# Performance work log

Hardware: AMD Instinct MI355X
Metric: run time of the kernel (lower is better)

Reference implementation:

```python
import jax, jax.numpy as jnp
import numpy as np

B, S, T = 128, 128, 128
E, H = 256, 512
NEG_INF = -1e9


def setup_inputs() -> dict:
    key = jax.random.key(0)
    ks = jax.random.split(key, 12)
    rn = lambda k, sh: (jax.random.normal(k, sh, jnp.float32) * 0.05)
    return {
        "trg_embed": rn(ks[0], (B, T, E)),
        "encoder_hidden": rn(ks[1], (B, S, 2 * H)),
        "encoder_final": rn(ks[2], (1, B, 2 * H)),
        "src_mask": jnp.ones((B, 1, S), bool),
        "trg_mask": jnp.ones((B, T), bool),
        # Bahdanau attention params (Linear, bias=False)
        "W_key": rn(ks[3], (H, 2 * H)),      # key_layer
        "W_query": rn(ks[4], (H, H)),        # query_layer
        "v_energy": rn(ks[5], (H,)),         # energy_layer (H -> 1)
        # GRU cell params (torch layout: gates [r, z, n])
        "W_ih": rn(ks[6], (3 * H, E + 2 * H)),
        "W_hh": rn(ks[7], (3 * H, H)),
        "b_ih": rn(ks[8], (3 * H,)),
        "b_hh": rn(ks[9], (3 * H,)),
        # bridge: Linear(2H -> H, bias=True)
        "W_bridge": rn(ks[10], (H, 2 * H)),
        "b_bridge": jnp.zeros((H,), jnp.float32),
        # pre_output_layer: Linear(H + 2H + E -> H, bias=False)
        "W_preout": rn(ks[11], (H, H + 2 * H + E)),
    }


def reference(trg_embed, encoder_hidden, encoder_final, src_mask, trg_mask,
              W_key, W_query, v_energy, W_ih, W_hh, b_ih, b_hh,
              W_bridge, b_bridge, W_preout):
    # proj_key precomputed once, as in the torch module
    proj_key = jnp.einsum("bsk,hk->bsh", encoder_hidden, W_key)  # [B,S,H]
    # init_hidden: tanh(bridge(encoder_final)); num_layers=1 -> h: [B,H]
    h0 = jnp.tanh(encoder_final[0] @ W_bridge.T + b_bridge)
    mask = src_mask[:, 0, :]  # [B,S]

    def step(h, prev_embed):  # h: [B,H], prev_embed: [B,E]
        # Bahdanau additive attention, query = last-layer hidden
        q = h @ W_query.T  # [B,H]
        scores = jnp.einsum("bsh,h->bs", jnp.tanh(q[:, None, :] + proj_key), v_energy)
        scores = jnp.where(mask, scores, NEG_INF)
        alphas = jax.nn.softmax(scores, axis=-1)
        context = jnp.einsum("bs,bsd->bd", alphas, encoder_hidden)  # [B,2H]
        # single-step GRU (torch gate order r, z, n)
        x = jnp.concatenate([prev_embed, context], axis=-1)  # [B,E+2H]
        gi = x @ W_ih.T + b_ih
        gh = h @ W_hh.T + b_hh
        i_r, i_z, i_n = jnp.split(gi, 3, axis=-1)
        h_r, h_z, h_n = jnp.split(gh, 3, axis=-1)
        r = jax.nn.sigmoid(i_r + h_r)
        z = jax.nn.sigmoid(i_z + h_z)
        n = jnp.tanh(i_n + r * h_n)
        h_new = (1.0 - z) * n + z * h
        # pre-output projection (dropout p=0 / eval mode)
        pre = jnp.concatenate([prev_embed, h_new, context], axis=-1) @ W_preout.T
        return h_new, (h_new, pre)

    xs = jnp.swapaxes(trg_embed, 0, 1)  # [T,B,E]
    hT, (states, preouts) = jax.lax.scan(step, h0, xs)
    decoder_states = jnp.swapaxes(states, 0, 1)      # [B,T,H]
    pre_output_vectors = jnp.swapaxes(preouts, 0, 1)  # [B,T,H]
    hidden = hT[None]  # [1,B,H] to mirror torch layout
    cell_state = jnp.zeros_like(hidden)  # GRU: untouched zeros
    return decoder_states, hidden, pre_output_vectors, cell_state
```

## Files before the change

### kernel.cpp

```cpp
#include <hip/hip_runtime.h>
#include <hip/hip_bf16.h>

typedef __bf16 bf16_t;
typedef __bf16 bf16x8 __attribute__((ext_vector_type(8)));
typedef float  f32x4  __attribute__((ext_vector_type(4)));
typedef float  f32x2  __attribute__((ext_vector_type(2)));

#define Bx 128
#define Sx 128
#define Tx 128
#define Ex 256
#define Hx 512
#define H2 1024
#define G3 1536
#define KX 1280
#define KP 1792

#define OUT_STATES 0
#define OUT_HID    8388608
#define OUT_PRE    8454144
#define OUT_CELL   16842752

__device__ __forceinline__ float fast_tanh(float x){
  float e = __expf(2.0f*x);
  return 1.0f - 2.0f/(e + 1.0f);
}
__device__ __forceinline__ float fast_sigmoid(float x){
  return 1.0f/(1.0f + __expf(-x));
}

__device__ __forceinline__ bf16x8 ld_cvt8(const float* p){
  f32x4 a = *(const f32x4*)p;
  f32x4 b = *(const f32x4*)(p+4);
  bf16x8 r;
  r[0]=(bf16_t)a[0]; r[1]=(bf16_t)a[1]; r[2]=(bf16_t)a[2]; r[3]=(bf16_t)a[3];
  r[4]=(bf16_t)b[0]; r[5]=(bf16_t)b[1]; r[6]=(bf16_t)b[2]; r[7]=(bf16_t)b[3];
  return r;
}

__device__ __forceinline__ f32x4 gemm_tile_bb(const bf16_t* A, int lda,
                                              const bf16_t* W, int ldw, int K, int lane){
  const int quad = lane >> 4, c = lane & 15;
  const bf16_t* pa = A + c*lda + quad*8;
  const bf16_t* pb = W + c*ldw + quad*8;
  f32x4 acc = {0.f,0.f,0.f,0.f};
  for (int k = 0; k < K; k += 32)
    acc = __builtin_amdgcn_mfma_f32_16x16x32_bf16(*(const bf16x8*)(pa+k),
                                                  *(const bf16x8*)(pb+k), acc, 0, 0, 0);
  return acc;
}

__device__ __forceinline__ void store_tile_f32(float* C, int ldc, f32x4 acc, int lane){
  const int quad = lane >> 4, c = lane & 15;
  #pragma unroll
  for (int r = 0; r < 4; r++) C[(quad*4 + r)*ldc + c] = acc[r];
}

__global__ void cvt_kernel(const float* __restrict__ in, bf16_t* __restrict__ out, int n){
  const int i = (blockIdx.x*256 + threadIdx.x)*4;
  if (i < n){
    f32x4 v = *(const f32x4*)(in + i);
    bf16_t o[4]; o[0]=(bf16_t)v[0]; o[1]=(bf16_t)v[1]; o[2]=(bf16_t)v[2]; o[3]=(bf16_t)v[3];
    *(ulong1*)(out + i) = *(ulong1*)o;
  }
}

__global__ void bridge_kernel(const float* __restrict__ ef, const float* __restrict__ Wb,
                              const float* __restrict__ bb,
                              float* __restrict__ hf, bf16_t* __restrict__ hb){
  const int b = blockIdx.x;
  const int h = threadIdx.x;
  __shared__ float efs[H2];
  for (int k = threadIdx.x; k < H2; k += blockDim.x) efs[k] = ef[b*H2 + k];
  __syncthreads();
  const float* wrow = Wb + h*H2;
  float acc = bb[h];
  for (int k = 0; k < H2; k += 4){
    f32x4 w = *(const f32x4*)(wrow + k);
    acc += efs[k]*w[0] + efs[k+1]*w[1] + efs[k+2]*w[2] + efs[k+3]*w[3];
  }
  float v = fast_tanh(acc);
  hf[b*Hx + h] = v;
  hb[b*Hx + h] = (bf16_t)v;
}

__global__ void pk_gemm(const float* __restrict__ eh, const bf16_t* __restrict__ Wkb,
                        bf16_t* __restrict__ pk){
  const int gwid = (blockIdx.x*blockDim.x + threadIdx.x) >> 6;
  const int lane = threadIdx.x & 63;
  const int quad = lane >> 4, c = lane & 15;
  const int mt = gwid >> 5;
  const int nt = gwid & 31;
  const float*  pa = eh  + (mt*16 + c)*H2 + quad*8;
  const bf16_t* pb = Wkb + (nt*16 + c)*H2 + quad*8;
  f32x4 acc = {0.f,0.f,0.f,0.f};
  for (int k = 0; k < H2; k += 32)
    acc = __builtin_amdgcn_mfma_f32_16x16x32_bf16(ld_cvt8(pa + k),
                                                  *(const bf16x8*)(pb + k), acc, 0,0,0);
  bf16_t* C = pk + mt*16*Hx + nt*16;
  #pragma unroll
  for (int r = 0; r < 4; r++) C[(quad*4 + r)*Hx + c] = (bf16_t)acc[r];
}

__global__ void __launch_bounds__(256)
p1_kernel(const bf16_t* __restrict__ hb, const bf16_t* __restrict__ Wqb,
          const bf16_t* __restrict__ Whhb, float* __restrict__ qf, float* __restrict__ ghf){
  const int lane = threadIdx.x & 63;
  const int gw = blockIdx.x*4 + (threadIdx.x >> 6);
  if (gw < 256){
    const int mt = gw >> 5, nt = gw & 31;
    f32x4 acc = gemm_tile_bb(hb + mt*16*Hx, Hx, Wqb + nt*16*Hx, Hx, Hx, lane);
    store_tile_f32(qf + mt*16*Hx + nt*16, Hx, acc, lane);
  } else {
    const int idx = gw - 256;
    const int mt = idx/96, nt = idx%96;
    f32x4 acc = gemm_tile_bb(hb + mt*16*Hx, Hx, Whhb + nt*16*Hx, Hx, Hx, lane);
    store_tile_f32(ghf + mt*16*G3 + nt*16, G3, acc, lane);
  }
}

__global__ void __launch_bounds__(256)
p2_kernel(const float* __restrict__ trg, const float* __restrict__ eh,
          const float* __restrict__ ven, const bf16_t* __restrict__ pk,
          const float* __restrict__ qf, bf16_t* __restrict__ xbuf, int t){
  const int tid  = threadIdx.x;
  const int lane = tid & 63;
  const int wid  = tid >> 6;
  const int b    = blockIdx.x >> 1;
  const int half = blockIdx.x & 1;

  __shared__ float sc[Sx];
  __shared__ float smax_s, ssum_s;

  float qv[8], vv[8];
  #pragma unroll
  for (int i = 0; i < 8; i++){
    qv[i] = qf[b*Hx + i*64 + lane];
    vv[i] = ven[i*64 + lane];
  }
  for (int j = 0; j < 32; j++){
    const int s = wid*32 + j;
    const bf16_t* row = pk + (b*Sx + s)*Hx;
    float p = 0.f;
    #pragma unroll
    for (int i = 0; i < 8; i++)
      p += fast_tanh(qv[i] + (float)row[i*64 + lane])*vv[i];
    #pragma unroll
    for (int o = 32; o; o >>= 1) p += __shfl_xor(p, o, 64);
    if (lane == 0) sc[s] = p;
  }
  __syncthreads();
  if (tid < 64){
    float m = fmaxf(sc[tid], sc[tid+64]);
    #pragma unroll
    for (int o = 32; o; o >>= 1) m = fmaxf(m, __shfl_xor(m, o, 64));
    if (tid == 0) smax_s = m;
  }
  __syncthreads();
  if (tid < 128) sc[tid] = __expf(sc[tid] - smax_s);
  __syncthreads();
  if (tid < 64){
    float ssum = sc[tid] + sc[tid+64];
    #pragma unroll
    for (int o = 32; o; o >>= 1) ssum += __shfl_xor(ssum, o, 64);
    if (tid == 0) ssum_s = ssum;
  }
  __syncthreads();
  const float inv = 1.0f/ssum_s;
  const int d0 = half*Hx + tid*2;
  const float* ehb = eh + b*Sx*H2;
  float c0 = 0.f, c1 = 0.f;
  #pragma unroll 4
  for (int s = 0; s < Sx; s++){
    const float a = sc[s];
    f32x2 v = *(const f32x2*)(ehb + s*H2 + d0);
    c0 += a*v[0];
    c1 += a*v[1];
  }
  c0 *= inv; c1 *= inv;
  bf16_t cb[2]; cb[0] = (bf16_t)c0; cb[1] = (bf16_t)c1;
  *(uint1*)(xbuf + b*KX + Ex + d0) = *(uint1*)cb;
  if (half == 0) xbuf[b*KX + tid] = (bf16_t)trg[(b*Tx + t)*Ex + tid];
}

__global__ void __launch_bounds__(256)
p3_kernel(const bf16_t* __restrict__ Wihb, const float* __restrict__ bih,
          const float* __restrict__ bhh, const bf16_t* __restrict__ Wpb,
          const bf16_t* __restrict__ xbuf, const float* __restrict__ ghf,
          float* __restrict__ hf, bf16_t* __restrict__ hb,
          float* __restrict__ states, float* __restrict__ pre, int t){
  const int lane = threadIdx.x & 63;
  const int gw = blockIdx.x*4 + (threadIdx.x >> 6);
  const int quad = lane >> 4, c16 = lane & 15;

  if (gw < 256){
    const int mt = gw >> 5, ntp = gw & 31;
    const bf16_t* A  = xbuf + (mt*16 + c16)*KX + quad*8;
    const bf16_t* B0 = Wihb + (ntp*16 + c16)*KX + quad*8;
    const bf16_t* B1 = B0 + Hx*KX;
    const bf16_t* B2 = B0 + H2*KX;
    f32x4 ar = {0.f,0.f,0.f,0.f}, az = ar, an = ar;
    for (int k = 0; k < KX; k += 32){
      bf16x8 a = *(const bf16x8*)(A + k);
      ar = __builtin_amdgcn_mfma_f32_16x16x32_bf16(a, *(const bf16x8*)(B0+k), ar, 0,0,0);
      az = __builtin_amdgcn_mfma_f32_16x16x32_bf16(a, *(const bf16x8*)(B1+k), az, 0,0,0);
      an = __builtin_amdgcn_mfma_f32_16x16x32_bf16(a, *(const bf16x8*)(B2+k), an, 0,0,0);
    }
    const int j = ntp*16 + c16;
    const float bir = bih[j], biz = bih[Hx+j], bin = bih[H2+j];
    const float bhr = bhh[j], bhz = bhh[Hx+j], bhn = bhh[H2+j];
    #pragma unroll
    for (int r = 0; r < 4; r++){
      const int b_ = mt*16 + quad*4 + r;
      const float hr = ghf[b_*G3 + j]       + bhr;
      const float hz = ghf[b_*G3 + Hx + j]  + bhz;
      const float hn = ghf[b_*G3 + H2 + j]  + bhn;
      const float rg = fast_sigmoid(ar[r] + bir + hr);
      const float zg = fast_sigmoid(az[r] + biz + hz);
      const float ng = fast_tanh(an[r] + bin + rg*hn);
      const float hold = hf[b_*Hx + j];
      const float hnew = (1.0f - zg)*ng + zg*hold;
      hf[b_*Hx + j] = hnew;
      hb[b_*Hx + j] = (bf16_t)hnew;
      states[(b_*Tx + t)*Hx + j] = hnew;
    }
  } else {
    const int idx = gw - 256;
    const int mt2 = idx >> 5, nt2 = idx & 31;
    const bf16_t* A = xbuf + (mt2*16 + c16)*KX + Ex + quad*8;
    const bf16_t* B = Wpb + (nt2*16 + c16)*KP + (Ex + Hx) + quad*8;
    f32x4 acc = {0.f,0.f,0.f,0.f};
    for (int k = 0; k < H2; k += 32)
      acc = __builtin_amdgcn_mfma_f32_16x16x32_bf16(*(const bf16x8*)(A+k),
                                                    *(const bf16x8*)(B+k), acc, 0,0,0);
    #pragma unroll
    for (int r = 0; r < 4; r++){
      const int b_ = mt2*16 + quad*4 + r;
      pre[(b_*Tx + t)*Hx + nt2*16 + c16] = acc[r];
    }
  }
}

__global__ void preout_gemm(const bf16_t* __restrict__ trgb, const float* __restrict__ states,
                            const bf16_t* __restrict__ Wpb, float* __restrict__ pre){
  const int gwid = (blockIdx.x*blockDim.x + threadIdx.x) >> 6;
  const int lane = threadIdx.x & 63;
  const int quad = lane >> 4, c16 = lane & 15;
  const int mt = gwid >> 5, nt = gwid & 31;
  const int m = mt*16 + c16;
  const bf16_t* Bp = Wpb + (nt*16 + c16)*KP + quad*8;
  f32x4 acc = {0.f,0.f,0.f,0.f};
  const bf16_t* Ae = trgb + m*Ex + quad*8;
  for (int k = 0; k < Ex; k += 32)
    acc = __builtin_amdgcn_mfma_f32_16x16x32_bf16(*(const bf16x8*)(Ae+k),
                                                  *(const bf16x8*)(Bp+k), acc, 0,0,0);
  const float* As = states + m*Hx + quad*8;
  for (int k = 0; k < Hx; k += 32)
    acc = __builtin_amdgcn_mfma_f32_16x16x32_bf16(ld_cvt8(As+k),
                                                  *(const bf16x8*)(Bp+Ex+k), acc, 0,0,0);
  float* C = pre + mt*16*Hx + nt*16;
  #pragma unroll
  for (int r = 0; r < 4; r++){
    const int o = (quad*4 + r)*Hx + c16;
    C[o] = acc[r] + C[o];
  }
}

__global__ void finalize_kernel(const float* __restrict__ hf,
                                float* __restrict__ hid, float* __restrict__ cell){
  const int i = blockIdx.x*256 + threadIdx.x;
  hid[i]  = hf[i];
  cell[i] = 0.0f;
}

extern "C" void kernel_launch(void* const* d_in, const int* in_sizes, int n_in,
                              void* d_out, int out_size, void* d_ws, size_t ws_size,
                              hipStream_t stream){
  int shift = 0;
  for (int i = 0; i < n_in; i++){
    if (in_sizes[i] == 1966080){ shift = i - 8; break; }
  }
  #define IN(k) (((k) < 3) ? d_in[(k)] : d_in[(k) + shift])
  const float* trg = (const float*)IN(0);
  const float* eh  = (const float*)IN(1);
  const float* ef  = (const float*)IN(2);
  const float* Wk  = (const float*)IN(5);
  const float* Wq  = (const float*)IN(6);
  const float* ven = (const float*)IN(7);
  const float* Wih = (const float*)IN(8);
  const float* Whh = (const float*)IN(9);
  const float* bih = (const float*)IN(10);
  const float* bhh = (const float*)IN(11);
  const float* Wb  = (const float*)IN(12);
  const float* bb  = (const float*)IN(13);
  const float* Wp  = (const float*)IN(14);
  #undef IN

  char* ws = (char*)d_ws;
  bf16_t* xbuf = (bf16_t*)(ws + 0);
  float*  hf   = (float* )(ws + 327680);
  bf16_t* hb   = (bf16_t*)(ws + 589824);
  float*  qf   = (float* )(ws + 720896);
  float*  ghf  = (float* )(ws + 983040);
  bf16_t* Wkb  = (bf16_t*)(ws + 1769472);
  bf16_t* Wqb  = (bf16_t*)(ws + 2818048);
  bf16_t* Whhb = (bf16_t*)(ws + 3342336);
  bf16_t* Wihb = (bf16_t*)(ws + 4915200);
  bf16_t* Wpb  = (bf16_t*)(ws + 8847360);
  bf16_t* trgb = (bf16_t*)(ws + 10682368);
  bf16_t* pk   = (bf16_t*)(ws + 19070976);

  float* out    = (float*)d_out;
  float* states = out + OUT_STATES;
  float* hid    = out + OUT_HID;
  float* pre    = out + OUT_PRE;
  float* cell   = out + OUT_CELL;

  cvt_kernel<<<dim3(512),  dim3(256), 0, stream>>>(Wk,  Wkb,  524288);
  cvt_kernel<<<dim3(256),  dim3(256), 0, stream>>>(Wq,  Wqb,  262144);
  cvt_kernel<<<dim3(768),  dim3(256), 0, stream>>>(Whh, Whhb, 786432);
  cvt_kernel<<<dim3(1920), dim3(256), 0, stream>>>(Wih, Wihb, 1966080);
  cvt_kernel<<<dim3(896),  dim3(256), 0, stream>>>(Wp,  Wpb,  917504);
  cvt_kernel<<<dim3(4096), dim3(256), 0, stream>>>(trg, trgb, 4194304);

  bridge_kernel<<<dim3(Bx), dim3(Hx), 0, stream>>>(ef, Wb, bb, hf, hb);
  pk_gemm<<<dim3(8192), dim3(256), 0, stream>>>(eh, Wkb, pk);

  for (int t = 0; t < Tx; t++){
    p1_kernel<<<dim3(256), dim3(256), 0, stream>>>(hb, Wqb, Whhb, qf, ghf);
    p2_kernel<<<dim3(256), dim3(256), 0, stream>>>(trg, eh, ven, pk, qf, xbuf, t);
    p3_kernel<<<dim3(128), dim3(256), 0, stream>>>(Wihb, bih, bhh, Wpb, xbuf, ghf,
                                                   hf, hb, states, pre, t);
  }

  preout_gemm<<<dim3(8192), dim3(256), 0, stream>>>(trgb, states, Wpb, pre);
  finalize_kernel<<<dim3(256), dim3(256), 0, stream>>>(hf, hid, cell);
}
```

Baseline: 9.239 ms.

## Fuse per-timestep kernels into one persistent cooperative scan kernel

```diff
diff --git a/kernel.cpp b/kernel.cpp
--- a/kernel.cpp
+++ b/kernel.cpp
@@ -1,8 +1,12 @@
 #include <hip/hip_runtime.h>
 #include <hip/hip_bf16.h>
+#include <hip/hip_cooperative_groups.h>
+
+namespace cg = cooperative_groups;
 
 typedef __bf16 bf16_t;
 typedef __bf16 bf16x8 __attribute__((ext_vector_type(8)));
+typedef __bf16 bf16x2 __attribute__((ext_vector_type(2)));
 typedef float  f32x4  __attribute__((ext_vector_type(4)));
 typedef float  f32x2  __attribute__((ext_vector_type(2)));
 
@@ -84,164 +88,189 @@
   hb[b*Hx + h] = (bf16_t)v;
 }
 
-__global__ void pk_gemm(const float* __restrict__ eh, const bf16_t* __restrict__ Wkb,
+__global__ void pk_gemm(const float* __restrict__ eh, const bf16_t* __restrict__ ehb,
+                        int use_ehb, const bf16_t* __restrict__ Wkb,
                         bf16_t* __restrict__ pk){
   const int gwid = (blockIdx.x*blockDim.x + threadIdx.x) >> 6;
   const int lane = threadIdx.x & 63;
   const int quad = lane >> 4, c = lane & 15;
   const int mt = gwid >> 5;
   const int nt = gwid & 31;
-  const float*  pa = eh  + (mt*16 + c)*H2 + quad*8;
   const bf16_t* pb = Wkb + (nt*16 + c)*H2 + quad*8;
   f32x4 acc = {0.f,0.f,0.f,0.f};
-  for (int k = 0; k < H2; k += 32)
-    acc = __builtin_amdgcn_mfma_f32_16x16x32_bf16(ld_cvt8(pa + k),
-                                                  *(const bf16x8*)(pb + k), acc, 0,0,0);
+  if (use_ehb){
+    const bf16_t* pa = ehb + (size_t)(mt*16 + c)*H2 + quad*8;
+    for (int k = 0; k < H2; k += 32)
+      acc = __builtin_amdgcn_mfma_f32_16x16x32_bf16(*(const bf16x8*)(pa+k),
+                                                    *(const bf16x8*)(pb+k), acc, 0,0,0);
+  } else {
+    const float* pa = eh + (size_t)(mt*16 + c)*H2 + quad*8;
+    for (int k = 0; k < H2; k += 32)
+      acc = __builtin_amdgcn_mfma_f32_16x16x32_bf16(ld_cvt8(pa+k),
+                                                    *(const bf16x8*)(pb+k), acc, 0,0,0);
+  }
   bf16_t* C = pk + mt*16*Hx + nt*16;
   #pragma unroll
   for (int r = 0; r < 4; r++) C[(quad*4 + r)*Hx + c] = (bf16_t)acc[r];
 }
 
 __global__ void __launch_bounds__(256)
-p1_kernel(const bf16_t* __restrict__ hb, const bf16_t* __restrict__ Wqb,
-          const bf16_t* __restrict__ Whhb, float* __restrict__ qf, float* __restrict__ ghf){
-  const int lane = threadIdx.x & 63;
-  const int gw = blockIdx.x*4 + (threadIdx.x >> 6);
-  if (gw < 256){
-    const int mt = gw >> 5, nt = gw & 31;
-    f32x4 acc = gemm_tile_bb(hb + mt*16*Hx, Hx, Wqb + nt*16*Hx, Hx, Hx, lane);
-    store_tile_f32(qf + mt*16*Hx + nt*16, Hx, acc, lane);
-  } else {
-    const int idx = gw - 256;
-    const int mt = idx/96, nt = idx%96;
-    f32x4 acc = gemm_tile_bb(hb + mt*16*Hx, Hx, Whhb + nt*16*Hx, Hx, Hx, lane);
-    store_tile_f32(ghf + mt*16*G3 + nt*16, G3, acc, lane);
-  }
-}
-
-__global__ void __launch_bounds__(256)
-p2_kernel(const float* __restrict__ trg, const float* __restrict__ eh,
-          const float* __restrict__ ven, const bf16_t* __restrict__ pk,
-          const float* __restrict__ qf, bf16_t* __restrict__ xbuf, int t){
+scan_kernel(const float* __restrict__ trg, const float* __restrict__ eh,
+            const bf16_t* __restrict__ ehb, int use_ehb,
+            const float* __restrict__ ven,
+            const bf16_t* __restrict__ Wqb, const bf16_t* __restrict__ Whhb,
+            const bf16_t* __restrict__ Wihb, const bf16_t* __restrict__ Wpb,
+            const float* __restrict__ bih, const float* __restrict__ bhh,
+            const bf16_t* __restrict__ pk, bf16_t* __restrict__ xbuf,
+            float* __restrict__ hf, bf16_t* __restrict__ hb,
+            float* __restrict__ qf, float* __restrict__ ghf,
+            float* __restrict__ states, float* __restrict__ pre){
+  cg::grid_group grid = cg::this_grid();
   const int tid  = threadIdx.x;
   const int lane = tid & 63;
   const int wid  = tid >> 6;
+  const int gw   = blockIdx.x*4 + wid;
+  const int quad = lane >> 4, c16 = lane & 15;
   const int b    = blockIdx.x >> 1;
   const int half = blockIdx.x & 1;
 
   __shared__ float sc[Sx];
   __shared__ float smax_s, ssum_s;
 
-  float qv[8], vv[8];
+  float vv[8];
   #pragma unroll
-  for (int i = 0; i < 8; i++){
-    qv[i] = qf[b*Hx + i*64 + lane];
-    vv[i] = ven[i*64 + lane];
-  }
-  for (int j = 0; j < 32; j++){
-    const int s = wid*32 + j;
-    const bf16_t* row = pk + (b*Sx + s)*Hx;
-    float p = 0.f;
-    #pragma unroll
-    for (int i = 0; i < 8; i++)
-      p += fast_tanh(qv[i] + (float)row[i*64 + lane])*vv[i];
-    #pragma unroll
-    for (int o = 32; o; o >>= 1) p += __shfl_xor(p, o, 64);
-    if (lane == 0) sc[s] = p;
-  }
-  __syncthreads();
-  if (tid < 64){
-    float m = fmaxf(sc[tid], sc[tid+64]);
-    #pragma unroll
-    for (int o = 32; o; o >>= 1) m = fmaxf(m, __shfl_xor(m, o, 64));
-    if (tid == 0) smax_s = m;
-  }
-  __syncthreads();
-  if (tid < 128) sc[tid] = __expf(sc[tid] - smax_s);
-  __syncthreads();
-  if (tid < 64){
-    float ssum = sc[tid] + sc[tid+64];
-    #pragma unroll
-    for (int o = 32; o; o >>= 1) ssum += __shfl_xor(ssum, o, 64);
-    if (tid == 0) ssum_s = ssum;
-  }
-  __syncthreads();
-  const float inv = 1.0f/ssum_s;
-  const int d0 = half*Hx + tid*2;
-  const float* ehb = eh + b*Sx*H2;
-  float c0 = 0.f, c1 = 0.f;
-  #pragma unroll 4
-  for (int s = 0; s < Sx; s++){
-    const float a = sc[s];
-    f32x2 v = *(const f32x2*)(ehb + s*H2 + d0);
-    c0 += a*v[0];
-    c1 += a*v[1];
-  }
-  c0 *= inv; c1 *= inv;
-  bf16_t cb[2]; cb[0] = (bf16_t)c0; cb[1] = (bf16_t)c1;
-  *(uint1*)(xbuf + b*KX + Ex + d0) = *(uint1*)cb;
-  if (half == 0) xbuf[b*KX + tid] = (bf16_t)trg[(b*Tx + t)*Ex + tid];
-}
-
-__global__ void __launch_bounds__(256)
-p3_kernel(const bf16_t* __restrict__ Wihb, const float* __restrict__ bih,
-          const float* __restrict__ bhh, const bf16_t* __restrict__ Wpb,
-          const bf16_t* __restrict__ xbuf, const float* __restrict__ ghf,
-          float* __restrict__ hf, bf16_t* __restrict__ hb,
-          float* __restrict__ states, float* __restrict__ pre, int t){
-  const int lane = threadIdx.x & 63;
-  const int gw = blockIdx.x*4 + (threadIdx.x >> 6);
-  const int quad = lane >> 4, c16 = lane & 15;
-
+  for (int i = 0; i < 8; i++) vv[i] = ven[lane*8 + i];
+
+  const int jP3 = (gw & 31)*16 + c16;
+  float bir=0.f,biz=0.f,bin=0.f,bhr=0.f,bhz=0.f,bhn=0.f;
   if (gw < 256){
-    const int mt = gw >> 5, ntp = gw & 31;
-    const bf16_t* A  = xbuf + (mt*16 + c16)*KX + quad*8;
-    const bf16_t* B0 = Wihb + (ntp*16 + c16)*KX + quad*8;
-    const bf16_t* B1 = B0 + Hx*KX;
-    const bf16_t* B2 = B0 + H2*KX;
-    f32x4 ar = {0.f,0.f,0.f,0.f}, az = ar, an = ar;
-    for (int k = 0; k < KX; k += 32){
-      bf16x8 a = *(const bf16x8*)(A + k);
-      ar = __builtin_amdgcn_mfma_f32_16x16x32_bf16(a, *(const bf16x8*)(B0+k), ar, 0,0,0);
-      az = __builtin_amdgcn_mfma_f32_16x16x32_bf16(a, *(const bf16x8*)(B1+k), az, 0,0,0);
-      an = __builtin_amdgcn_mfma_f32_16x16x32_bf16(a, *(const bf16x8*)(B2+k), an, 0,0,0);
+    bir=bih[jP3]; biz=bih[Hx+jP3]; bin=bih[H2+jP3];
+    bhr=bhh[jP3]; bhz=bhh[Hx+jP3]; bhn=bhh[H2+jP3];
+  }
+
+  for (int t = 0; t < Tx; t++){
+    if (gw < 256){
+      const int mt = gw >> 5, nt = gw & 31;
+      f32x4 acc = gemm_tile_bb(hb + mt*16*Hx, Hx, Wqb + nt*16*Hx, Hx, Hx, lane);
+      store_tile_f32(qf + mt*16*Hx + nt*16, Hx, acc, lane);
+    } else {
+      const int idx = gw - 256;
+      const int mt = idx/96, nt = idx%96;
+      f32x4 acc = gemm_tile_bb(hb + mt*16*Hx, Hx, Whhb + nt*16*Hx, Hx, Hx, lane);
+      store_tile_f32(ghf + mt*16*G3 + nt*16, G3, acc, lane);
     }
-    const int j = ntp*16 + c16;
-    const float bir = bih[j], biz = bih[Hx+j], bin = bih[H2+j];
-    const float bhr = bhh[j], bhz = bhh[Hx+j], bhn = bhh[H2+j];
-    #pragma unroll
-    for (int r = 0; r < 4; r++){
-      const int b_ = mt*16 + quad*4 + r;
-      const float hr = ghf[b_*G3 + j]       + bhr;
-      const float hz = ghf[b_*G3 + Hx + j]  + bhz;
-      const float hn = ghf[b_*G3 + H2 + j]  + bhn;
-      const float rg = fast_sigmoid(ar[r] + bir + hr);
-      const float zg = fast_sigmoid(az[r] + biz + hz);
-      const float ng = fast_tanh(an[r] + bin + rg*hn);
-      const float hold = hf[b_*Hx + j];
-      const float hnew = (1.0f - zg)*ng + zg*hold;
-      hf[b_*Hx + j] = hnew;
-      hb[b_*Hx + j] = (bf16_t)hnew;
-      states[(b_*Tx + t)*Hx + j] = hnew;
+    grid.sync();
+
+    {
+      float qv[8];
+      #pragma unroll
+      for (int i = 0; i < 8; i++) qv[i] = qf[b*Hx + lane*8 + i];
+      for (int j = 0; j < 32; j++){
+        const int s = wid*32 + j;
+        bf16x8 pv = *(const bf16x8*)(pk + (size_t)(b*Sx + s)*Hx + lane*8);
+        float p = 0.f;
+        #pragma unroll
+        for (int i = 0; i < 8; i++)
+          p += fast_tanh(qv[i] + (float)pv[i])*vv[i];
+        #pragma unroll
+        for (int o = 32; o; o >>= 1) p += __shfl_xor(p, o, 64);
+        if (lane == 0) sc[s] = p;
+      }
+      __syncthreads();
+      if (tid < 64){
+        float m = fmaxf(sc[tid], sc[tid+64]);
+        #pragma unroll
+        for (int o = 32; o; o >>= 1) m = fmaxf(m, __shfl_xor(m, o, 64));
+        if (tid == 0) smax_s = m;
+      }
+      __syncthreads();
+      if (tid < 128) sc[tid] = __expf(sc[tid] - smax_s);
+      __syncthreads();
+      if (tid < 64){
+        float ssum = sc[tid] + sc[tid+64];
+        #pragma unroll
+        for (int o = 32; o; o >>= 1) ssum += __shfl_xor(ssum, o, 64);
+        if (tid == 0) ssum_s = ssum;
+      }
+      __syncthreads();
+      const float inv = 1.0f/ssum_s;
+      const int d0 = half*Hx + tid*2;
+      float c0 = 0.f, c1 = 0.f;
+      if (use_ehb){
+        const bf16_t* p0 = ehb + (size_t)b*Sx*H2 + d0;
+        #pragma unroll 8
+        for (int s = 0; s < Sx; s++){
+          const float a = sc[s];
+          bf16x2 v = *(const bf16x2*)(p0 + (size_t)s*H2);
+          c0 += a*(float)v[0];
+          c1 += a*(float)v[1];
+        }
+      } else {
+        const float* p0 = eh + (size_t)b*Sx*H2 + d0;
+        #pragma unroll 8
+        for (int s = 0; s < Sx; s++){
+          const float a = sc[s];
+          f32x2 v = *(const f32x2*)(p0 + (size_t)s*H2);
+          c0 += a*v[0];
+          c1 += a*v[1];
+        }
+      }
+      c0 *= inv; c1 *= inv;
+      bf16x2 cb; cb[0] = (bf16_t)c0; cb[1] = (bf16_t)c1;
+      *(bf16x2*)(xbuf + b*KX + Ex + d0) = cb;
+      if (half == 0) xbuf[b*KX + tid] = (bf16_t)trg[(b*Tx + t)*Ex + tid];
     }
-  } else {
-    const int idx = gw - 256;
-    const int mt2 = idx >> 5, nt2 = idx & 31;
-    const bf16_t* A = xbuf + (mt2*16 + c16)*KX + Ex + quad*8;
-    const bf16_t* B = Wpb + (nt2*16 + c16)*KP + (Ex + Hx) + quad*8;
-    f32x4 acc = {0.f,0.f,0.f,0.f};
-    for (int k = 0; k < H2; k += 32)
-      acc = __builtin_amdgcn_mfma_f32_16x16x32_bf16(*(const bf16x8*)(A+k),
-                                                    *(const bf16x8*)(B+k), acc, 0,0,0);
-    #pragma unroll
-    for (int r = 0; r < 4; r++){
-      const int b_ = mt2*16 + quad*4 + r;
-      pre[(b_*Tx + t)*Hx + nt2*16 + c16] = acc[r];
+    grid.sync();
+
+    if (gw < 256){
+      const int mt = gw >> 5, ntp = gw & 31;
+      const bf16_t* A  = xbuf + (mt*16 + c16)*KX + quad*8;
+      const bf16_t* B0 = Wihb + (ntp*16 + c16)*KX + quad*8;
+      const bf16_t* B1 = B0 + Hx*KX;
+      const bf16_t* B2 = B0 + H2*KX;
+      f32x4 ar = {0.f,0.f,0.f,0.f}, az = ar, an = ar;
+      for (int k = 0; k < KX; k += 32){
+        bf16x8 a = *(const bf16x8*)(A + k);
+        ar = __builtin_amdgcn_mfma_f32_16x16x32_bf16(a, *(const bf16x8*)(B0+k), ar, 0,0,0);
+        az = __builtin_amdgcn_mfma_f32_16x16x32_bf16(a, *(const bf16x8*)(B1+k), az, 0,0,0);
+        an = __builtin_amdgcn_mfma_f32_16x16x32_bf16(a, *(const bf16x8*)(B2+k), an, 0,0,0);
+      }
+      const int j = jP3;
+      #pragma unroll
+      for (int r = 0; r < 4; r++){
+        const int b_ = mt*16 + quad*4 + r;
+        const float hr = ghf[b_*G3 + j]       + bhr;
+        const float hz = ghf[b_*G3 + Hx + j]  + bhz;
+        const float hn = ghf[b_*G3 + H2 + j]  + bhn;
+        const float rg = fast_sigmoid(ar[r] + bir + hr);
+        const float zg = fast_sigmoid(az[r] + biz + hz);
+        const float ng = fast_tanh(an[r] + bin + rg*hn);
+        const float hold = hf[b_*Hx + j];
+        const float hnew = (1.0f - zg)*ng + zg*hold;
+        hf[b_*Hx + j] = hnew;
+        hb[b_*Hx + j] = (bf16_t)hnew;
+        states[(size_t)(b_*Tx + t)*Hx + j] = hnew;
+      }
+    } else if (gw < 512){
+      const int idx = gw - 256;
+      const int mt2 = idx >> 5, nt2 = idx & 31;
+      const bf16_t* A = xbuf + (mt2*16 + c16)*KX + Ex + quad*8;
+      const bf16_t* B = Wpb + (nt2*16 + c16)*KP + (Ex + Hx) + quad*8;
+      f32x4 acc = {0.f,0.f,0.f,0.f};
+      for (int k = 0; k < H2; k += 32)
+        acc = __builtin_amdgcn_mfma_f32_16x16x32_bf16(*(const bf16x8*)(A+k),
+                                                      *(const bf16x8*)(B+k), acc, 0,0,0);
+      #pragma unroll
+      for (int r = 0; r < 4; r++){
+        const int b_ = mt2*16 + quad*4 + r;
+        pre[(size_t)(b_*Tx + t)*Hx + nt2*16 + c16] = acc[r];
+      }
     }
-  }
-}
-
-__global__ void preout_gemm(const bf16_t* __restrict__ trgb, const float* __restrict__ states,
+    grid.sync();
+  }
+}
+
+__global__ void preout_gemm(const float* __restrict__ trg, const float* __restrict__ states,
                             const bf16_t* __restrict__ Wpb, float* __restrict__ pre){
   const int gwid = (blockIdx.x*blockDim.x + threadIdx.x) >> 6;
   const int lane = threadIdx.x & 63;
@@ -250,11 +279,11 @@
   const int m = mt*16 + c16;
   const bf16_t* Bp = Wpb + (nt*16 + c16)*KP + quad*8;
   f32x4 acc = {0.f,0.f,0.f,0.f};
-  const bf16_t* Ae = trgb + m*Ex + quad*8;
+  const float* Ae = trg + (size_t)m*Ex + quad*8;
   for (int k = 0; k < Ex; k += 32)
-    acc = __builtin_amdgcn_mfma_f32_16x16x32_bf16(*(const bf16x8*)(Ae+k),
+    acc = __builtin_amdgcn_mfma_f32_16x16x32_bf16(ld_cvt8(Ae+k),
                                                   *(const bf16x8*)(Bp+k), acc, 0,0,0);
-  const float* As = states + m*Hx + quad*8;
+  const float* As = states + (size_t)m*Hx + quad*8;
   for (int k = 0; k < Hx; k += 32)
     acc = __builtin_amdgcn_mfma_f32_16x16x32_bf16(ld_cvt8(As+k),
                                                   *(const bf16x8*)(Bp+Ex+k), acc, 0,0,0);
@@ -302,13 +331,14 @@
   bf16_t* hb   = (bf16_t*)(ws + 589824);
   float*  qf   = (float* )(ws + 720896);
   float*  ghf  = (float* )(ws + 983040);
-  bf16_t* Wkb  = (bf16_t*)(ws + 1769472);
-  bf16_t* Wqb  = (bf16_t*)(ws + 2818048);
-  bf16_t* Whhb = (bf16_t*)(ws + 3342336);
-  bf16_t* Wihb = (bf16_t*)(ws + 4915200);
-  bf16_t* Wpb  = (bf16_t*)(ws + 8847360);
-  bf16_t* trgb = (bf16_t*)(ws + 10682368);
-  bf16_t* pk   = (bf16_t*)(ws + 19070976);
+  bf16_t* Wqb  = (bf16_t*)(ws + 1769472);
+  bf16_t* Whhb = (bf16_t*)(ws + 2293760);
+  bf16_t* Wihb = (bf16_t*)(ws + 3866624);
+  bf16_t* Wpb  = (bf16_t*)(ws + 7798784);
+  bf16_t* Wkb  = (bf16_t*)(ws + 9633792);
+  bf16_t* pk   = (bf16_t*)(ws + 10682368);
+  bf16_t* ehb  = (bf16_t*)(ws + 27459584);
+  const int use_ehb = (ws_size >= (size_t)61014016) ? 1 : 0;
 
   float* out    = (float*)d_out;
   float* states = out + OUT_STATES;
@@ -316,23 +346,26 @@
   float* pre    = out + OUT_PRE;
   float* cell   = out + OUT_CELL;
 
-  cvt_kernel<<<dim3(512),  dim3(256), 0, stream>>>(Wk,  Wkb,  524288);
   cvt_kernel<<<dim3(256),  dim3(256), 0, stream>>>(Wq,  Wqb,  262144);
   cvt_kernel<<<dim3(768),  dim3(256), 0, stream>>>(Whh, Whhb, 786432);
   cvt_kernel<<<dim3(1920), dim3(256), 0, stream>>>(Wih, Wihb, 1966080);
   cvt_kernel<<<dim3(896),  dim3(256), 0, stream>>>(Wp,  Wpb,  917504);
-  cvt_kernel<<<dim3(4096), dim3(256), 0, stream>>>(trg, trgb, 4194304);
+  cvt_kernel<<<dim3(512),  dim3(256), 0, stream>>>(Wk,  Wkb,  524288);
+  if (use_ehb)
+    cvt_kernel<<<dim3(16384), dim3(256), 0, stream>>>(eh, ehb, 16777216);
 
   bridge_kernel<<<dim3(Bx), dim3(Hx), 0, stream>>>(ef, Wb, bb, hf, hb);
-  pk_gemm<<<dim3(8192), dim3(256), 0, stream>>>(eh, Wkb, pk);
-
-  for (int t = 0; t < Tx; t++){
-    p1_kernel<<<dim3(256), dim3(256), 0, stream>>>(hb, Wqb, Whhb, qf, ghf);
-    p2_kernel<<<dim3(256), dim3(256), 0, stream>>>(trg, eh, ven, pk, qf, xbuf, t);
-    p3_kernel<<<dim3(128), dim3(256), 0, stream>>>(Wihb, bih, bhh, Wpb, xbuf, ghf,
-                                                   hf, hb, states, pre, t);
-  }
-
-  preout_gemm<<<dim3(8192), dim3(256), 0, stream>>>(trgb, states, Wpb, pre);
+  pk_gemm<<<dim3(8192), dim3(256), 0, stream>>>(eh, ehb, use_ehb, Wkb, pk);
+
+  int use_ehb_k = use_ehb;
+  void* args[] = {(void*)&trg, (void*)&eh, (void*)&ehb, (void*)&use_ehb_k,
+                  (void*)&ven, (void*)&Wqb, (void*)&Whhb, (void*)&Wihb, (void*)&Wpb,
+                  (void*)&bih, (void*)&bhh, (void*)&pk, (void*)&xbuf,
+                  (void*)&hf, (void*)&hb, (void*)&qf, (void*)&ghf,
+                  (void*)&states, (void*)&pre};
+  hipLaunchCooperativeKernel((const void*)scan_kernel, dim3(256), dim3(256),
+                             args, 0, stream);
+
+  preout_gemm<<<dim3(8192), dim3(256), 0, stream>>>(trg, states, Wpb, pre);
   finalize_kernel<<<dim3(256), dim3(256), 0, stream>>>(hf, hid, cell);
 }
```

Result: slower. 27.57 ms (+198.5%).
